# Kernel optimization log

Measured on AMD Instinct MI355X. Metric: run time of the kernel, lower is better.

Reference implementation:

```python
import jax, jax.numpy as jnp
import numpy as np
import math

WINDOW_SIZE = 11
SIGMA = 1.5
CHANNELS = 3
C1 = 0.01 ** 2
C2 = 0.03 ** 2
PAD = WINDOW_SIZE // 2


def make_window():
    # 1D gaussian, normalized, then outer product -> (C, 1, K, K) depthwise kernel
    xs = np.arange(WINDOW_SIZE)
    g = np.exp(-((xs - WINDOW_SIZE // 2) ** 2) / (2.0 * SIGMA ** 2))
    g = (g / g.sum()).astype(np.float32)
    w2d = np.outer(g, g)  # (K, K)
    w = np.broadcast_to(w2d[None, None], (CHANNELS, 1, WINDOW_SIZE, WINDOW_SIZE))
    return jnp.asarray(np.ascontiguousarray(w))


def _dwconv(x, window):
    # depthwise conv2d, groups = channels, 'same' padding for odd K
    return jax.lax.conv_general_dilated(
        x, window,
        window_strides=(1, 1),
        padding=[(PAD, PAD), (PAD, PAD)],
        dimension_numbers=("NCHW", "OIHW", "NCHW"),
        feature_group_count=CHANNELS,
    )


def _ssim_loss(img1, img2, window):
    mu1 = _dwconv(img1, window)
    mu2 = _dwconv(img2, window)
    mu1_sq = mu1 * mu1
    mu2_sq = mu2 * mu2
    mu1_mu2 = mu1 * mu2
    sigma1_sq = _dwconv(img1 * img1, window) - mu1_sq
    sigma2_sq = _dwconv(img2 * img2, window) - mu2_sq
    sigma12 = _dwconv(img1 * img2, window) - mu1_mu2
    ssim_map = ((2.0 * mu1_mu2 + C1) * (2.0 * sigma12 + C2)) / (
        (mu1_sq + mu2_sq + C1) * (sigma1_sq + sigma2_sq + C2)
    )
    return 1.0 - jnp.mean(ssim_map)  # reduction='mean'


def setup_inputs() -> dict:
    key = jax.random.key(0)
    k1, k2 = jax.random.split(key)
    B, C, H, W = 4, 3, 1088, 1920
    img1 = jax.random.uniform(k1, (B, C, H, W), dtype=jnp.float32)
    img2 = jax.random.uniform(k2, (B, C, H, W), dtype=jnp.float32)
    window = make_window()
    return {"img1": img1, "img2": img2, "window": window}


def reference(img1, img2, window):
    return _ssim_loss(img1, img2, window)
```

## Files before the change

### kernel.cpp

```cpp
#include <hip/hip_runtime.h>


typedef _Float16 half8  __attribute__((ext_vector_type(8)));
typedef float    f32x4  __attribute__((ext_vector_type(4)));
typedef unsigned int uint4v __attribute__((ext_vector_type(4)));

namespace {
constexpr int IW  = 1920;
constexpr int IH  = 1088;
constexpr int NPL = 12;
constexpr int TW  = 16;
constexpr int TH  = 64;
constexpr int TX  = IW / TW;
constexpr int TY  = IH / TH;
constexpr int NTILE = TX * TY * NPL;
constexpr int NSLOT = 128;
constexpr int SPAD  = 8;
constexpr float C1v = 0.0001f;
constexpr float C2v = 0.0009f;
constexpr double NPIX = 25067520.0;
}

__global__ __launch_bounds__(256)
__attribute__((amdgpu_waves_per_eu(3, 8)))
void ssim_main(const float* __restrict__ img1,
               const float* __restrict__ img2,
               double* __restrict__ acc) {
    const int lane = threadIdx.x & 63;
    const int wv   = threadIdx.x >> 6;
    const int wid  = blockIdx.x * 4 + wv;

    const int tx = wid % TX;
    const int t2 = wid / TX;
    const int ty = t2 % TY;
    const int pl = t2 / TY;

    const int l15 = lane & 15;
    const int lg  = lane >> 4;

    const int X0  = tx * TW;
    const int gx0 = X0 - 8 + lg * 8;

    const float* __restrict__ base1 = img1 + (long long)pl * IH * IW;
    const float* __restrict__ base2 = img2 + (long long)pl * IH * IW;

    half8 wH, wV;
#pragma unroll
    for (int i = 0; i < 8; ++i) {
        const int k   = lg * 8 + i;
        const int iv  = k - l15;
        const int ih2 = iv - 3;
        const int dv = iv - 5, dh = ih2 - 5;
        const float ev = __expf((float)(dv * dv) * (-1.0f / 4.5f)) * 0.26601172f;
        const float eh = __expf((float)(dh * dh) * (-1.0f / 4.5f)) * 0.26601172f;
        wV[i] = (_Float16)((iv  >= 0 && iv  <= 10) ? ev : 0.0f);
        wH[i] = (_Float16)((ih2 >= 0 && ih2 <= 10) ? eh : 0.0f);
    }

    float sum = 0.0f;
    const f32x4 zz = {0.0f, 0.0f, 0.0f, 0.0f};

    f32x4 pA[2][2][2], pB[2][2][2];

    auto issue_loads = [&](int g, int par) {
        const int Yb = ty * TH + g * 16 - 5;
        const bool safe = (tx > 0) && (tx < TX - 1) &&
                          !(ty == 0 && g == 0) && !(ty == TY - 1 && g == 3);
#pragma unroll
        for (int c = 0; c < 2; ++c) {
            const int rr = Yb + ((l15 >> 2) * 8 + c * 4 + (l15 & 3));
            const long long rb = (long long)rr * IW;
            if (safe) {
                const f32x4* pa = (const f32x4*)(base1 + rb + gx0);
                const f32x4* pb = (const f32x4*)(base2 + rb + gx0);
                pA[par][c][0] = pa[0]; pA[par][c][1] = pa[1];
                pB[par][c][0] = pb[0]; pB[par][c][1] = pb[1];
            } else {
                const bool rok = (unsigned)rr < (unsigned)IH;
#pragma unroll
                for (int j = 0; j < 2; ++j) {
                    f32x4 va = zz, vb = zz;
                    if (rok) {
#pragma unroll
                        for (int e = 0; e < 4; ++e) {
                            const int gx = gx0 + 4 * j + e;
                            if (gx >= 0 && gx < IW) {
                                va[e] = base1[rb + gx];
                                vb[e] = base2[rb + gx];
                            }
                        }
                    }
                    pA[par][c][j] = va;
                    pB[par][c][j] = vb;
                }
            }
        }
    };

    auto pack8 = [](f32x4 u, f32x4 v) -> half8 {
        uint4v t;
        t[0] = __builtin_bit_cast(unsigned int, __builtin_amdgcn_cvt_pkrtz(u[0], u[1]));
        t[1] = __builtin_bit_cast(unsigned int, __builtin_amdgcn_cvt_pkrtz(u[2], u[3]));
        t[2] = __builtin_bit_cast(unsigned int, __builtin_amdgcn_cvt_pkrtz(v[0], v[1]));
        t[3] = __builtin_bit_cast(unsigned int, __builtin_amdgcn_cvt_pkrtz(v[2], v[3]));
        return __builtin_bit_cast(half8, t);
    };

    issue_loads(0, 0);
    issue_loads(1, 1);

#pragma unroll
    for (int g = 0; g < 4; ++g) {
        const int par = g & 1;

        const half8 af0 = pack8(pA[par][0][0], pA[par][0][1]);
        const half8 bf0 = pack8(pB[par][0][0], pB[par][0][1]);
        const half8 af1 = pack8(pA[par][1][0], pA[par][1][1]);
        const half8 bf1 = pack8(pB[par][1][0], pB[par][1][1]);

        if (g < 2) issue_loads(g + 2, par);

        f32x4 cA, cB;
        cA = __builtin_amdgcn_mfma_f32_16x16x32_f16(af0, wH, zz, 0, 0, 0);
        cB = __builtin_amdgcn_mfma_f32_16x16x32_f16(af1, wH, zz, 0, 0, 0);
        const half8 h0 = pack8(cA, cB);
        cA = __builtin_amdgcn_mfma_f32_16x16x32_f16(bf0, wH, zz, 0, 0, 0);
        cB = __builtin_amdgcn_mfma_f32_16x16x32_f16(bf1, wH, zz, 0, 0, 0);
        const half8 h1 = pack8(cA, cB);
        cA = __builtin_amdgcn_mfma_f32_16x16x32_f16(af0 * af0, wH, zz, 0, 0, 0);
        cB = __builtin_amdgcn_mfma_f32_16x16x32_f16(af1 * af1, wH, zz, 0, 0, 0);
        const half8 h2 = pack8(cA, cB);
        cA = __builtin_amdgcn_mfma_f32_16x16x32_f16(bf0 * bf0, wH, zz, 0, 0, 0);
        cB = __builtin_amdgcn_mfma_f32_16x16x32_f16(bf1 * bf1, wH, zz, 0, 0, 0);
        const half8 h3 = pack8(cA, cB);
        cA = __builtin_amdgcn_mfma_f32_16x16x32_f16(af0 * bf0, wH, zz, 0, 0, 0);
        cB = __builtin_amdgcn_mfma_f32_16x16x32_f16(af1 * bf1, wH, zz, 0, 0, 0);
        const half8 h4 = pack8(cA, cB);

        const f32x4 a0 = __builtin_amdgcn_mfma_f32_16x16x32_f16(wV, h0, zz, 0, 0, 0);
        const f32x4 a1 = __builtin_amdgcn_mfma_f32_16x16x32_f16(wV, h1, zz, 0, 0, 0);
        const f32x4 a2 = __builtin_amdgcn_mfma_f32_16x16x32_f16(wV, h2, zz, 0, 0, 0);
        const f32x4 a3 = __builtin_amdgcn_mfma_f32_16x16x32_f16(wV, h3, zz, 0, 0, 0);
        const f32x4 a4 = __builtin_amdgcn_mfma_f32_16x16x32_f16(wV, h4, zz, 0, 0, 0);

#pragma unroll
        for (int i = 0; i < 4; ++i) {
            const float mu1 = a0[i], mu2 = a1[i];
            const float ea = a2[i], eb = a3[i], eab = a4[i];
            const float mu1s = mu1 * mu1, mu2s = mu2 * mu2, mu12 = mu1 * mu2;
            const float s1 = ea - mu1s, s2 = eb - mu2s, s12 = eab - mu12;
            const float num = (2.0f * mu12 + C1v) * (2.0f * s12 + C2v);
            const float den = (mu1s + mu2s + C1v) * (s1 + s2 + C2v);
            sum += num * __builtin_amdgcn_rcpf(den);
        }
    }

#pragma unroll
    for (int off = 32; off > 0; off >>= 1) sum += __shfl_down(sum, off);

    __shared__ double bsum[4];
    if (lane == 0) bsum[wv] = (double)sum;
    __syncthreads();
    if (threadIdx.x == 0) {
        const double s = bsum[0] + bsum[1] + bsum[2] + bsum[3];
        atomicAdd(acc + (blockIdx.x & (NSLOT - 1)) * SPAD, s);
    }
}

__global__ void ssim_fin(const double* __restrict__ acc, float* __restrict__ out) {
    const int lane = threadIdx.x & 63;
    double s = acc[lane * SPAD] + acc[(lane + 64) * SPAD];
#pragma unroll
    for (int off = 32; off > 0; off >>= 1)
        s += __shfl_down(s, off);
    if (lane == 0) out[0] = 1.0f - (float)(s / NPIX);
}

extern "C" void kernel_launch(void* const* d_in, const int* in_sizes, int n_in,
                              void* d_out, int out_size, void* d_ws, size_t ws_size,
                              hipStream_t stream) {
    (void)in_sizes; (void)n_in; (void)out_size; (void)ws_size;
    const float* img1 = (const float*)d_in[0];
    const float* img2 = (const float*)d_in[1];
    float* out = (float*)d_out;
    double* acc = (double*)d_ws;

    (void)hipMemsetAsync(acc, 0, NSLOT * SPAD * sizeof(double), stream);
    ssim_main<<<dim3(NTILE / 4), dim3(256), 0, stream>>>(img1, img2, acc);
    ssim_fin<<<1, 64, 0, stream>>>(acc, out);
}
```

Baseline: 293.1 us.

## Process six horizontal tiles per wave with loads pipelined across tiles

Each wave now walks a strip of six adjacent 16x64 tiles instead of one, and issues the next tile's first loads while the current tile's last groups are computing. The goal is to amortize per-wave setup (weight generation, reduction, atomic) and keep memory loads in flight across tile boundaries. In exchange the grid shrinks sixfold (NSTRIP/4 = 1020 blocks), which may hurt occupancy and load balance. Tile halos are still reloaded per tile, not shared.

```diff
diff --git a/kernel.cpp b/kernel.cpp
--- a/kernel.cpp
+++ b/kernel.cpp
@@ -11,9 +11,10 @@
 constexpr int NPL = 12;
 constexpr int TW  = 16;
 constexpr int TH  = 64;
-constexpr int TX  = IW / TW;
+constexpr int TPS = 6;
+constexpr int SX  = IW / (TW * TPS);
 constexpr int TY  = IH / TH;
-constexpr int NTILE = TX * TY * NPL;
+constexpr int NSTRIP = SX * TY * NPL;
 constexpr int NSLOT = 128;
 constexpr int SPAD  = 8;
 constexpr float C1v = 0.0001f;
@@ -30,16 +31,13 @@
     const int wv   = threadIdx.x >> 6;
     const int wid  = blockIdx.x * 4 + wv;
 
-    const int tx = wid % TX;
-    const int t2 = wid / TX;
-    const int ty = t2 % TY;
-    const int pl = t2 / TY;
+    const int sx = wid % SX;
+    const int s2 = wid / SX;
+    const int ty = s2 % TY;
+    const int pl = s2 / TY;
 
     const int l15 = lane & 15;
     const int lg  = lane >> 4;
-
-    const int X0  = tx * TW;
-    const int gx0 = X0 - 8 + lg * 8;
 
     const float* __restrict__ base1 = img1 + (long long)pl * IH * IW;
     const float* __restrict__ base2 = img2 + (long long)pl * IH * IW;
@@ -62,9 +60,11 @@
 
     f32x4 pA[2][2][2], pB[2][2][2];
 
-    auto issue_loads = [&](int g, int par) {
-        const int Yb = ty * TH + g * 16 - 5;
-        const bool safe = (tx > 0) && (tx < TX - 1) &&
+    auto issue_loads = [&](int t, int g, int par) {
+        const int tx  = sx * TPS + t;
+        const int gx0 = tx * TW - 8 + lg * 8;
+        const int Yb  = ty * TH + g * 16 - 5;
+        const bool safe = (tx > 0) && (tx < IW / TW - 1) &&
                           !(ty == 0 && g == 0) && !(ty == TY - 1 && g == 3);
 #pragma unroll
         for (int c = 0; c < 2; ++c) {
@@ -106,52 +106,59 @@
         return __builtin_bit_cast(half8, t);
     };
 
-    issue_loads(0, 0);
-    issue_loads(1, 1);
+    issue_loads(0, 0, 0);
+    issue_loads(0, 1, 1);
+
+#pragma clang loop unroll(disable)
+    for (int t = 0; t < TPS; ++t) {
+#pragma unroll
+        for (int g = 0; g < 4; ++g) {
+            const int par = g & 1;
+
+            const half8 af0 = pack8(pA[par][0][0], pA[par][0][1]);
+            const half8 bf0 = pack8(pB[par][0][0], pB[par][0][1]);
+            const half8 af1 = pack8(pA[par][1][0], pA[par][1][1]);
+            const half8 bf1 = pack8(pB[par][1][0], pB[par][1][1]);
+
+            if (g < 2) {
+                issue_loads(t, g + 2, par);
+            } else if (t < TPS - 1) {
+                issue_loads(t + 1, g - 2, par);
+            }
+
+            f32x4 cA, cB;
+            cA = __builtin_amdgcn_mfma_f32_16x16x32_f16(af0, wH, zz, 0, 0, 0);
+            cB = __builtin_amdgcn_mfma_f32_16x16x32_f16(af1, wH, zz, 0, 0, 0);
+            const half8 h0 = pack8(cA, cB);
+            cA = __builtin_amdgcn_mfma_f32_16x16x32_f16(bf0, wH, zz, 0, 0, 0);
+            cB = __builtin_amdgcn_mfma_f32_16x16x32_f16(bf1, wH, zz, 0, 0, 0);
+            const half8 h1 = pack8(cA, cB);
+            cA = __builtin_amdgcn_mfma_f32_16x16x32_f16(af0 * af0, wH, zz, 0, 0, 0);
+            cB = __builtin_amdgcn_mfma_f32_16x16x32_f16(af1 * af1, wH, zz, 0, 0, 0);
+            const half8 h2 = pack8(cA, cB);
+            cA = __builtin_amdgcn_mfma_f32_16x16x32_f16(bf0 * bf0, wH, zz, 0, 0, 0);
+            cB = __builtin_amdgcn_mfma_f32_16x16x32_f16(bf1 * bf1, wH, zz, 0, 0, 0);
+            const half8 h3 = pack8(cA, cB);
+            cA = __builtin_amdgcn_mfma_f32_16x16x32_f16(af0 * bf0, wH, zz, 0, 0, 0);
+            cB = __builtin_amdgcn_mfma_f32_16x16x32_f16(af1 * bf1, wH, zz, 0, 0, 0);
+            const half8 h4 = pack8(cA, cB);
+
+            const f32x4 a0 = __builtin_amdgcn_mfma_f32_16x16x32_f16(wV, h0, zz, 0, 0, 0);
+            const f32x4 a1 = __builtin_amdgcn_mfma_f32_16x16x32_f16(wV, h1, zz, 0, 0, 0);
+            const f32x4 a2 = __builtin_amdgcn_mfma_f32_16x16x32_f16(wV, h2, zz, 0, 0, 0);
+            const f32x4 a3 = __builtin_amdgcn_mfma_f32_16x16x32_f16(wV, h3, zz, 0, 0, 0);
+            const f32x4 a4 = __builtin_amdgcn_mfma_f32_16x16x32_f16(wV, h4, zz, 0, 0, 0);
 
 #pragma unroll
-    for (int g = 0; g < 4; ++g) {
-        const int par = g & 1;
-
-        const half8 af0 = pack8(pA[par][0][0], pA[par][0][1]);
-        const half8 bf0 = pack8(pB[par][0][0], pB[par][0][1]);
-        const half8 af1 = pack8(pA[par][1][0], pA[par][1][1]);
-        const half8 bf1 = pack8(pB[par][1][0], pB[par][1][1]);
-
-        if (g < 2) issue_loads(g + 2, par);
-
-        f32x4 cA, cB;
-        cA = __builtin_amdgcn_mfma_f32_16x16x32_f16(af0, wH, zz, 0, 0, 0);
-        cB = __builtin_amdgcn_mfma_f32_16x16x32_f16(af1, wH, zz, 0, 0, 0);
-        const half8 h0 = pack8(cA, cB);
-        cA = __builtin_amdgcn_mfma_f32_16x16x32_f16(bf0, wH, zz, 0, 0, 0);
-        cB = __builtin_amdgcn_mfma_f32_16x16x32_f16(bf1, wH, zz, 0, 0, 0);
-        const half8 h1 = pack8(cA, cB);
-        cA = __builtin_amdgcn_mfma_f32_16x16x32_f16(af0 * af0, wH, zz, 0, 0, 0);
-        cB = __builtin_amdgcn_mfma_f32_16x16x32_f16(af1 * af1, wH, zz, 0, 0, 0);
-        const half8 h2 = pack8(cA, cB);
-        cA = __builtin_amdgcn_mfma_f32_16x16x32_f16(bf0 * bf0, wH, zz, 0, 0, 0);
-        cB = __builtin_amdgcn_mfma_f32_16x16x32_f16(bf1 * bf1, wH, zz, 0, 0, 0);
-        const half8 h3 = pack8(cA, cB);
-        cA = __builtin_amdgcn_mfma_f32_16x16x32_f16(af0 * bf0, wH, zz, 0, 0, 0);
-        cB = __builtin_amdgcn_mfma_f32_16x16x32_f16(af1 * bf1, wH, zz, 0, 0, 0);
-        const half8 h4 = pack8(cA, cB);
-
-        const f32x4 a0 = __builtin_amdgcn_mfma_f32_16x16x32_f16(wV, h0, zz, 0, 0, 0);
-        const f32x4 a1 = __builtin_amdgcn_mfma_f32_16x16x32_f16(wV, h1, zz, 0, 0, 0);
-        const f32x4 a2 = __builtin_amdgcn_mfma_f32_16x16x32_f16(wV, h2, zz, 0, 0, 0);
-        const f32x4 a3 = __builtin_amdgcn_mfma_f32_16x16x32_f16(wV, h3, zz, 0, 0, 0);
-        const f32x4 a4 = __builtin_amdgcn_mfma_f32_16x16x32_f16(wV, h4, zz, 0, 0, 0);
-
-#pragma unroll
-        for (int i = 0; i < 4; ++i) {
-            const float mu1 = a0[i], mu2 = a1[i];
-            const float ea = a2[i], eb = a3[i], eab = a4[i];
-            const float mu1s = mu1 * mu1, mu2s = mu2 * mu2, mu12 = mu1 * mu2;
-            const float s1 = ea - mu1s, s2 = eb - mu2s, s12 = eab - mu12;
-            const float num = (2.0f * mu12 + C1v) * (2.0f * s12 + C2v);
-            const float den = (mu1s + mu2s + C1v) * (s1 + s2 + C2v);
-            sum += num * __builtin_amdgcn_rcpf(den);
+            for (int i = 0; i < 4; ++i) {
+                const float mu1 = a0[i], mu2 = a1[i];
+                const float ea = a2[i], eb = a3[i], eab = a4[i];
+                const float mu1s = mu1 * mu1, mu2s = mu2 * mu2, mu12 = mu1 * mu2;
+                const float s1 = ea - mu1s, s2v = eb - mu2s, s12 = eab - mu12;
+                const float num = (2.0f * mu12 + C1v) * (2.0f * s12 + C2v);
+                const float den = (mu1s + mu2s + C1v) * (s1 + s2v + C2v);
+                sum += num * __builtin_amdgcn_rcpf(den);
+            }
         }
     }
 
@@ -186,6 +193,6 @@
     double* acc = (double*)d_ws;
 
     (void)hipMemsetAsync(acc, 0, NSLOT * SPAD * sizeof(double), stream);
-    ssim_main<<<dim3(NTILE / 4), dim3(256), 0, stream>>>(img1, img2, acc);
+    ssim_main<<<dim3(NSTRIP / 4), dim3(256), 0, stream>>>(img1, img2, acc);
     ssim_fin<<<1, 64, 0, stream>>>(acc, out);
 }
```

Measured after the change: 448.9 us. 53.1% more time.
